# Performance work log

Hardware: AMD Instinct MI355X
Metric: run time of the kernel (lower is better)

The kernel has to match this reference:

```python
import jax, jax.numpy as jnp
import numpy as np

B, N, C = 16, 32768, 3
PRE, POST, IOU_THRESH = 4096, 512, 0.7


def setup_inputs() -> dict:
    key = jax.random.key(0)
    k1, k2, k3, k4 = jax.random.split(key, 4)
    centers = jax.random.uniform(k1, (B, N, 3), minval=0.0, maxval=70.0)
    sizes = jax.random.uniform(k2, (B, N, 3), minval=1.0, maxval=5.0)
    ry = jax.random.uniform(k3, (B, N, 1), minval=-np.pi, maxval=np.pi)
    batch_box_preds = jnp.concatenate([centers, sizes, ry], axis=-1)  # (B,N,7)
    batch_cls_preds = jax.random.uniform(k4, (B, N, C))  # normalized class scores
    return {"batch_box_preds": batch_box_preds, "batch_cls_preds": batch_cls_preds}


def _nms_single(boxes, scores):
    """Greedy class-agnostic NMS for one sample.
    boxes: (N,7) [x,y,z,dx,dy,dz,ry]; scores: (N,).
    Returns selected indices into the original N boxes and a validity mask,
    both of fixed length POST (padded).
    BEV IoU uses axis-aligned footprints (x,y,dx,dy)."""
    top_s, top_i = jax.lax.top_k(scores, PRE)  # pre-maxsize filtering by score
    tb = boxes[top_i]  # (PRE,7)
    x1 = tb[:, 0] - tb[:, 3] * 0.5
    x2 = tb[:, 0] + tb[:, 3] * 0.5
    y1 = tb[:, 1] - tb[:, 4] * 0.5
    y2 = tb[:, 1] + tb[:, 4] * 0.5
    area = (x2 - x1) * (y2 - y1)

    def step(active, _):
        ms = jnp.where(active, top_s, -jnp.inf)
        j = jnp.argmax(ms)
        valid = active[j]
        ix = jnp.clip(jnp.minimum(x2, x2[j]) - jnp.maximum(x1, x1[j]), 0.0)
        iy = jnp.clip(jnp.minimum(y2, y2[j]) - jnp.maximum(y1, y1[j]), 0.0)
        inter = ix * iy
        iou = inter / (area + area[j] - inter + 1e-8)
        # suppress overlapping boxes (j suppresses itself, iou==1)
        active = active & jnp.where(valid, iou < IOU_THRESH, True)
        return active, (jnp.where(valid, top_i[j], 0), valid)

    active0 = jnp.ones(PRE, dtype=bool)
    _, (sel_idx, sel_valid) = jax.lax.scan(step, active0, None, length=POST)
    return sel_idx, sel_valid


def reference(batch_box_preds, batch_cls_preds):
    # cur_roi_scores, cur_roi_labels = torch.max(cls_preds, dim=1)
    scores = jnp.max(batch_cls_preds, axis=-1)          # (B,N)
    labels = jnp.argmax(batch_cls_preds, axis=-1)       # (B,N)
    sel_idx, sel_valid = jax.vmap(_nms_single)(batch_box_preds, scores)  # (B,POST)
    gather = jax.vmap(lambda a, i: a[i])
    rois = jnp.where(sel_valid[..., None], gather(batch_box_preds, sel_idx), 0.0)  # (B,POST,7)
    roi_scores = jnp.where(sel_valid, gather(scores, sel_idx), 0.0)                # (B,POST)
    roi_labels = jnp.where(sel_valid, gather(labels, sel_idx), 0) + 1              # (B,POST), pad -> 1 as in torch code
    return rois, roi_scores, roi_labels
```

## Files before the change

### kernel.cpp

```cpp
#include <hip/hip_runtime.h>
#include <stdint.h>

#define BATCH 16
#define NBOX  32768
#define PRE   4096
#define POST  512

#define PADIDX(i) ((i) + ((i) >> 4))

typedef unsigned long long u64;
typedef unsigned int u32;
typedef unsigned short u16;

__device__ inline u64 shfl64(u64 v, int src) {
    int lo = __shfl((int)(v & 0xffffffffULL), src);
    int hi = __shfl((int)(v >> 32), src);
    return ((u64)(u32)hi << 32) | (u32)lo;
}

__global__ __launch_bounds__(1024) void k_sortkeys4096(const float* __restrict__ cls,
                                                       u64* __restrict__ out) {
    __shared__ u64 s[PRE + (PRE >> 4)];
    int g = blockIdx.x;
    u64* dst = out + (size_t)g * PRE;
    int tid = threadIdx.x;
    for (int i = tid; i < PRE; i += 1024) {
        int idx = g * PRE + i;
        const float* c = cls + (size_t)idx * 3;
        float sc = fmaxf(fmaxf(c[0], c[1]), c[2]);
        u32 sb = __float_as_uint(sc);
        s[PADIDX(i)] = ((u64)(~sb) << 32) | (u32)(idx & (NBOX - 1));
    }
    for (int k = 2; k <= PRE; k <<= 1) {
        for (int jj = k >> 1; jj > 0; jj >>= 1) {
            __syncthreads();
            for (int p = tid; p < PRE / 2; p += 1024) {
                int i = 2 * p - (p & (jj - 1));
                int l = i + jj;
                bool asc = ((i & k) == 0);
                u64 a = s[PADIDX(i)], b = s[PADIDX(l)];
                if ((a > b) == asc) { s[PADIDX(i)] = b; s[PADIDX(l)] = a; }
            }
        }
    }
    __syncthreads();
    for (int i = tid; i < PRE; i += 1024) dst[i] = s[PADIDX(i)];
}

__global__ __launch_bounds__(256) void k_mergepath(const u64* __restrict__ in,
                                                   u64* __restrict__ out, int npairs) {
    __shared__ u64 sA[PRE], sB[PRE];
    int b = blockIdx.x / npairs, p = blockIdx.x % npairs;
    const u64* A  = in + ((size_t)b * npairs * 2 + (size_t)p * 2) * PRE;
    const u64* Bp = A + PRE;
    u64* dst = out + ((size_t)b * npairs + p) * PRE;
    int tid = threadIdx.x;
    for (int i = tid; i < PRE; i += 256) { sA[i] = A[i]; sB[i] = Bp[i]; }
    __syncthreads();
    int d = tid * 16;
    int lo = d > PRE ? d - PRE : 0;
    int hi = d < PRE ? d : PRE;
    while (lo < hi) {
        int mid = (lo + hi) >> 1;
        if (sA[mid] < sB[d - 1 - mid]) lo = mid + 1; else hi = mid;
    }
    int a = lo, bi = d - lo;
    u64 av = a  < PRE ? sA[a]  : ~0ULL;
    u64 bv = bi < PRE ? sB[bi] : ~0ULL;
    u64 res[16];
    #pragma unroll
    for (int q = 0; q < 16; ++q) {
        bool ta = av < bv;
        res[q] = ta ? av : bv;
        if (ta) { ++a;  av = a  < PRE ? sA[a]  : ~0ULL; }
        else    { ++bi; bv = bi < PRE ? sB[bi] : ~0ULL; }
    }
    #pragma unroll
    for (int q = 0; q < 16; ++q) dst[d + q] = res[q];
}

__global__ __launch_bounds__(256) void k_coords(const u64* __restrict__ topkeys,
                                                const float* __restrict__ boxes,
                                                float* __restrict__ cx1,
                                                float* __restrict__ cy1,
                                                float* __restrict__ cx2,
                                                float* __restrict__ cy2,
                                                float* __restrict__ car) {
    int g = blockIdx.x * 256 + threadIdx.x;
    int b = g >> 12;
    u64 key = topkeys[g];
    int n = (int)(key & 0xffffffffULL);
    const float* bp = boxes + ((size_t)b * NBOX + n) * 7;
    float cx = bp[0], cy = bp[1], dx = bp[3], dy = bp[4];
    float hx = __fmul_rn(dx, 0.5f), hy = __fmul_rn(dy, 0.5f);
    float x1 = __fsub_rn(cx, hx), x2 = __fadd_rn(cx, hx);
    float y1 = __fsub_rn(cy, hy), y2 = __fadd_rn(cy, hy);
    cx1[g] = x1; cy1[g] = y1; cx2[g] = x2; cy2[g] = y2;
    car[g] = __fmul_rn(__fsub_rn(x2, x1), __fsub_rn(y2, y1));
}

__global__ __launch_bounds__(256) void k_iou(const float* __restrict__ cx1,
                                             const float* __restrict__ cy1,
                                             const float* __restrict__ cx2,
                                             const float* __restrict__ cy2,
                                             const float* __restrict__ car,
                                             u32* __restrict__ counts,
                                             u16* __restrict__ lists,
                                             u32* __restrict__ spcnt,
                                             u32* __restrict__ spill) {
    __shared__ float s1[64], s2[64], s3[64], s4[64], s5[64];
    int b = blockIdx.y;
    int t = blockIdx.x, blk = 0;
    while (t >= 64 - blk) { t -= 64 - blk; ++blk; }
    int wd = blk + t;
    size_t base = (size_t)b * PRE;
    int bb = b * PRE;
    int tid = threadIdx.x;
    if (tid < 64) {
        int i = blk * 64 + tid;
        s1[tid] = cx1[base + i]; s2[tid] = cy1[base + i];
        s3[tid] = cx2[base + i]; s4[tid] = cy2[base + i];
        s5[tid] = car[base + i];
    }
    __syncthreads();
    int w = tid >> 6, lane = tid & 63;
    int j = wd * 64 + lane;
    float jx1 = cx1[base + j], jy1 = cy1[base + j];
    float jx2 = cx2[base + j], jy2 = cy2[base + j];
    float ja  = car[base + j];
    const double M = (double)0.7f - 0x1p-25;
    int r0 = w * 16;
    #pragma unroll 4
    for (int r = 0; r < 16; ++r) {
        int i = blk * 64 + r0 + r;
        float rx1 = s1[r0 + r], ry1 = s2[r0 + r];
        float rx2 = s3[r0 + r], ry2 = s4[r0 + r], ra = s5[r0 + r];
        float ix = fmaxf(__fsub_rn(fminf(jx2, rx2), fmaxf(jx1, rx1)), 0.0f);
        float iy = fmaxf(__fsub_rn(fminf(jy2, ry2), fmaxf(jy1, ry1)), 0.0f);
        float inter = __fmul_rn(ix, iy);
        bool cand = (j > i) && (inter > 0.0f);
        u64 m = 0;
        if (__ballot(cand)) {
            float ssum = __fadd_rn(ja, ra);
            float d    = __fsub_rn(ssum, inter);
            float q    = __fadd_rn(d, 1e-8f);
            bool sup = cand && ((double)inter > M * (double)q);
            m = __ballot(sup);
        }
        if (lane == 0 && m) {
            u64 mm = m;
            while (mm) {
                int jj = __ffsll(mm) - 1; mm &= mm - 1;
                u32 slot = atomicAdd(&counts[bb + i], 1u);
                if (slot < 7)
                    lists[((size_t)(bb + i)) * 8 + 1 + slot] = (u16)(wd * 64 + jj);
                else {
                    u32 sp = atomicAdd(&spcnt[b], 1u);
                    if (sp < 4096) spill[(b << 12) + sp] = ((u32)i << 16) | (u32)(wd * 64 + jj);
                }
            }
        }
    }
}

__global__ __launch_bounds__(256) void k_walk(const u32* __restrict__ counts,
                                              const u16* __restrict__ lists,
                                              const u32* __restrict__ spcnt,
                                              const u32* __restrict__ spill,
                                              const u64* __restrict__ topkeys,
                                              const float* __restrict__ boxes,
                                              const float* __restrict__ cls,
                                              float* __restrict__ out) {
    __shared__ uint4 lrow[PRE];
    __shared__ u32   lbits[128];
    __shared__ u32   lspill[4096];
    __shared__ int   ssel[POST];
    __shared__ int   scnt, ssp;
    int b = blockIdx.x;
    int tid = threadIdx.x;
    const u64* keys = topkeys + (size_t)b * PRE;
    const uint4* listv = (const uint4*)(lists + ((size_t)b * PRE) * 8);

    if (tid < 128) lbits[tid] = 0;
    if (tid == 0) { u32 s = spcnt[b]; ssp = s > 4096u ? 4096 : (int)s; }
    __syncthreads();
    for (int i = tid; i < PRE; i += 256) {
        uint4 row = listv[i];
        u32 c = counts[b * PRE + i];
        row.x = (row.x & 0xFFFF0000u) | (c > 65535u ? 65535u : c);
        lrow[i] = row;
        if (c) atomicOr(&lbits[i >> 5], 1u << (i & 31));
    }
    __syncthreads();
    int spn = ssp;
    for (int q = tid; q < spn; q += 256) lspill[q] = spill[(b << 12) + q];
    __syncthreads();

    if (tid < 64) {
        int lane = tid;
        u64 act = ~0ULL;
        u64 hasl = ((u64)lbits[2 * lane + 1] << 32) | lbits[2 * lane];
        int cnt = 0;
        while (true) {
            u64 bal = __ballot(act != 0ULL);
            if (!bal) break;
            int fw = __ffsll(bal) - 1;
            u64 wsel = shfl64(act, fw);
            int i = (fw << 6) + __ffsll(wsel) - 1;
            if (lane == 0) ssel[cnt] = i;
            if (++cnt == POST) break;
            if (lane == fw) act &= ~(1ULL << (i & 63));
            u64 hb = shfl64(hasl, fw);
            if ((hb >> (i & 63)) & 1ULL) {
                uint4 row = lrow[i];
                int c = (int)(row.x & 0xFFFFu);
                u64 m = 0;
                int e;
                e = (int)(row.x >> 16);      if (c > 0 && (e >> 6) == lane) m |= 1ULL << (e & 63);
                e = (int)(row.y & 0xFFFFu);  if (c > 1 && (e >> 6) == lane) m |= 1ULL << (e & 63);
                e = (int)(row.y >> 16);      if (c > 2 && (e >> 6) == lane) m |= 1ULL << (e & 63);
                e = (int)(row.z & 0xFFFFu);  if (c > 3 && (e >> 6) == lane) m |= 1ULL << (e & 63);
                e = (int)(row.z >> 16);      if (c > 4 && (e >> 6) == lane) m |= 1ULL << (e & 63);
                e = (int)(row.w & 0xFFFFu);  if (c > 5 && (e >> 6) == lane) m |= 1ULL << (e & 63);
                e = (int)(row.w >> 16);      if (c > 6 && (e >> 6) == lane) m |= 1ULL << (e & 63);
                if (c > 7) {
                    for (int q = 0; q < spn; ++q) {
                        u32 en = lspill[q];
                        if ((int)(en >> 16) == i) {
                            int j2 = (int)(en & 0xFFFFu);
                            if ((j2 >> 6) == lane) m |= 1ULL << (j2 & 63);
                        }
                    }
                }
                act &= ~m;
            }
        }
        if (lane == 0) scnt = cnt;
    }
    __syncthreads();
    int cnt = scnt;
    for (int k = tid; k < POST; k += 256) if (k >= cnt) ssel[k] = -1;
    __syncthreads();

    const int R1 = BATCH * POST * 7;
    const int R2 = R1 + BATCH * POST;
    for (int k = tid; k < POST; k += 256) {
        int j = ssel[k];
        float* ro = out + ((size_t)b * POST + k) * 7;
        float score = 0.0f, labelf = 1.0f;
        if (j >= 0) {
            u64 key = keys[j];
            int n = (int)(key & 0xffffffffULL);
            const float* bp = boxes + ((size_t)b * NBOX + n) * 7;
            #pragma unroll
            for (int c = 0; c < 7; ++c) ro[c] = bp[c];
            score = __uint_as_float(~(u32)(key >> 32));
            const float* cp = cls + ((size_t)b * NBOX + n) * 3;
            float c0 = cp[0], c1 = cp[1], c2 = cp[2];
            int lab = 0; float best = c0;
            if (c1 > best) { best = c1; lab = 1; }
            if (c2 > best) { lab = 2; }
            labelf = (float)(lab + 1);
        } else {
            #pragma unroll
            for (int c = 0; c < 7; ++c) ro[c] = 0.0f;
        }
        out[R1 + b * POST + k] = score;
        out[R2 + b * POST + k] = labelf;
    }
}

__global__ __launch_bounds__(1024) void k_nms(const u64* __restrict__ topkeys,
                                              const float* __restrict__ boxes,
                                              const float* __restrict__ cls,
                                              float* __restrict__ out) {
    __shared__ float sx1[PRE], sy1[PRE], sx2[PRE], sy2[PRE], sarea[PRE];
    __shared__ int   sorig[PRE];
    __shared__ u64   smask[PRE / 64];
    __shared__ int   ssel[POST];
    __shared__ int   scur;
    int b = blockIdx.x;
    int tid = threadIdx.x;
    const u64* keys = topkeys + (size_t)b * PRE;

    for (int i = tid; i < PRE; i += 1024) {
        u64 key = keys[i];
        int n = (int)(key & 0xffffffffULL);
        sorig[i] = n;
        const float* bp = boxes + ((size_t)b * NBOX + n) * 7;
        float cx = bp[0], cy = bp[1], dx = bp[3], dy = bp[4];
        float hx = __fmul_rn(dx, 0.5f), hy = __fmul_rn(dy, 0.5f);
        float x1 = __fsub_rn(cx, hx), x2 = __fadd_rn(cx, hx);
        float y1 = __fsub_rn(cy, hy), y2 = __fadd_rn(cy, hy);
        sx1[i] = x1; sx2[i] = x2; sy1[i] = y1; sy2[i] = y2;
        sarea[i] = __fmul_rn(__fsub_rn(x2, x1), __fsub_rn(y2, y1));
    }
    if (tid < PRE / 64) smask[tid] = ~0ULL;
    __syncthreads();

    int lane = tid & 63;
    int wv   = tid >> 6;
    for (int r = 0; r < POST; ++r) {
        if (tid < 64) {
            u64 w = smask[lane];
            u64 nz = __ballot(w != 0ULL);
            int j = -1;
            if (nz) {
                int fw = __ffsll(nz) - 1;
                u64 wf = shfl64(w, fw);
                j = (fw << 6) + __ffsll(wf) - 1;
            }
            if (lane == 0) { scur = j; ssel[r] = j; }
        }
        __syncthreads();
        int j = scur;
        if (j < 0) {
            for (int k = r + tid; k < POST; k += 1024) ssel[k] = -1;
            __syncthreads();
            break;
        }
        float x1j = sx1[j], x2j = sx2[j], y1j = sy1[j], y2j = sy2[j], aj = sarea[j];
        for (int wd = wv * 4; wd < wv * 4 + 4; ++wd) {
            u64 m = smask[wd];
            if (m == 0ULL) continue;
            int i = (wd << 6) + lane;
            float ix = fmaxf(__fsub_rn(fminf(sx2[i], x2j), fmaxf(sx1[i], x1j)), 0.0f);
            float iy = fmaxf(__fsub_rn(fminf(sy2[i], y2j), fmaxf(sy1[i], y1j)), 0.0f);
            float inter = __fmul_rn(ix, iy);
            float denom = __fadd_rn(__fsub_rn(__fadd_rn(sarea[i], aj), inter), 1e-8f);
            float iou = __fdiv_rn(inter, denom);
            u64 clr = __ballot(!(iou < 0.7f));
            if (lane == 0) smask[wd] = m & ~clr;
        }
        __syncthreads();
    }

    const int R1 = BATCH * POST * 7;
    const int R2 = R1 + BATCH * POST;
    for (int k = tid; k < POST; k += 1024) {
        int j = ssel[k];
        float* ro = out + ((size_t)b * POST + k) * 7;
        float score = 0.0f, labelf = 1.0f;
        if (j >= 0) {
            int n = sorig[j];
            const float* bp = boxes + ((size_t)b * NBOX + n) * 7;
            #pragma unroll
            for (int c = 0; c < 7; ++c) ro[c] = bp[c];
            u64 key = keys[j];
            score = __uint_as_float(~(u32)(key >> 32));
            const float* cp = cls + ((size_t)b * NBOX + n) * 3;
            float c0 = cp[0], c1 = cp[1], c2 = cp[2];
            int lab = 0; float best = c0;
            if (c1 > best) { best = c1; lab = 1; }
            if (c2 > best) { lab = 2; }
            labelf = (float)(lab + 1);
        } else {
            #pragma unroll
            for (int c = 0; c < 7; ++c) ro[c] = 0.0f;
        }
        out[R1 + b * POST + k] = score;
        out[R2 + b * POST + k] = labelf;
    }
}

extern "C" void kernel_launch(void* const* d_in, const int* in_sizes, int n_in,
                              void* d_out, int out_size, void* d_ws, size_t ws_size,
                              hipStream_t stream) {
    const float* boxes = (const float*)d_in[0];
    const float* cls   = (const float*)d_in[1];
    float* out = (float*)d_out;

    char* ws = (char*)d_ws;
    u64*   keysA  = (u64*)(ws + 0);
    u64*   keysB  = (u64*)(ws + 4194304);
    float* cx1    = (float*)(ws + 8388608);
    float* cy1    = (float*)(ws + 8650752);
    float* cx2    = (float*)(ws + 8912896);
    float* cy2    = (float*)(ws + 9175040);
    float* car    = (float*)(ws + 9437184);
    u32*   counts = (u32*)(ws + 9699328);
    u32*   spcnt  = (u32*)(ws + 9961472);
    u32*   spill  = (u32*)(ws + 9961536);
    u16*   lists  = (u16*)(ws + 10223680);
    const size_t NEED = 10223680 + (size_t)BATCH * PRE * 8 * sizeof(u16);

    k_sortkeys4096<<<BATCH * 8, 1024, 0, stream>>>(cls, keysB);
    k_mergepath<<<BATCH * 4, 256, 0, stream>>>(keysB, keysA, 4);
    k_mergepath<<<BATCH * 2, 256, 0, stream>>>(keysA, keysB, 2);
    k_mergepath<<<BATCH, 256, 0, stream>>>(keysB, keysA, 1);

    if (ws_size >= NEED) {
        hipMemsetAsync(ws + 9699328, 0, 262208, stream);
        k_coords<<<(BATCH * PRE) / 256, 256, 0, stream>>>(keysA, boxes,
                                                          cx1, cy1, cx2, cy2, car);
        k_iou<<<dim3(2080, BATCH), 256, 0, stream>>>(cx1, cy1, cx2, cy2, car,
                                                     counts, lists, spcnt, spill);
        k_walk<<<BATCH, 256, 0, stream>>>(counts, lists, spcnt, spill,
                                          keysA, boxes, cls, out);
    } else {
        k_nms<<<BATCH, 1024, 0, stream>>>(keysA, boxes, cls, out);
    }
}
```

Before: 310.6 us.

## Run greedy NMS walk on a single thread with shared-memory suppression masks

The greedy selection walk moves from a 64-lane wavefront that used ballot and shuffle for every pick to one thread scanning 64-bit words of an active mask kept in LDS. Suppression inside the current word clears bits in a register, and suppression in later words uses atomicAnd on shared memory. The aim is to remove the per-iteration cross-lane ballot and shuffle latency in this serial loop. The cost is that one thread now does every step, and it takes a shared-memory round trip whenever a suppressed box lies in another word.

```diff
diff --git a/kernel.cpp b/kernel.cpp
--- a/kernel.cpp
+++ b/kernel.cpp
@@ -172,7 +172,8 @@
                                               const float* __restrict__ cls,
                                               float* __restrict__ out) {
     __shared__ uint4 lrow[PRE];
-    __shared__ u32   lbits[128];
+    __shared__ u64   smask[64];
+    __shared__ u64   haslw[64];
     __shared__ u32   lspill[4096];
     __shared__ int   ssel[POST];
     __shared__ int   scnt, ssp;
@@ -181,7 +182,7 @@
     const u64* keys = topkeys + (size_t)b * PRE;
     const uint4* listv = (const uint4*)(lists + ((size_t)b * PRE) * 8);
 
-    if (tid < 128) lbits[tid] = 0;
+    if (tid < 64) { smask[tid] = ~0ULL; haslw[tid] = 0ULL; }
     if (tid == 0) { u32 s = spcnt[b]; ssp = s > 4096u ? 4096 : (int)s; }
     __syncthreads();
     for (int i = tid; i < PRE; i += 256) {
@@ -189,53 +190,54 @@
         u32 c = counts[b * PRE + i];
         row.x = (row.x & 0xFFFF0000u) | (c > 65535u ? 65535u : c);
         lrow[i] = row;
-        if (c) atomicOr(&lbits[i >> 5], 1u << (i & 31));
+        if (c) atomicOr(&haslw[i >> 6], 1ULL << (i & 63));
     }
     __syncthreads();
     int spn = ssp;
     for (int q = tid; q < spn; q += 256) lspill[q] = spill[(b << 12) + q];
     __syncthreads();
 
-    if (tid < 64) {
-        int lane = tid;
-        u64 act = ~0ULL;
-        u64 hasl = ((u64)lbits[2 * lane + 1] << 32) | lbits[2 * lane];
+    if (tid == 0) {
         int cnt = 0;
-        while (true) {
-            u64 bal = __ballot(act != 0ULL);
-            if (!bal) break;
-            int fw = __ffsll(bal) - 1;
-            u64 wsel = shfl64(act, fw);
-            int i = (fw << 6) + __ffsll(wsel) - 1;
-            if (lane == 0) ssel[cnt] = i;
-            if (++cnt == POST) break;
-            if (lane == fw) act &= ~(1ULL << (i & 63));
-            u64 hb = shfl64(hasl, fw);
-            if ((hb >> (i & 63)) & 1ULL) {
-                uint4 row = lrow[i];
-                int c = (int)(row.x & 0xFFFFu);
-                u64 m = 0;
-                int e;
-                e = (int)(row.x >> 16);      if (c > 0 && (e >> 6) == lane) m |= 1ULL << (e & 63);
-                e = (int)(row.y & 0xFFFFu);  if (c > 1 && (e >> 6) == lane) m |= 1ULL << (e & 63);
-                e = (int)(row.y >> 16);      if (c > 2 && (e >> 6) == lane) m |= 1ULL << (e & 63);
-                e = (int)(row.z & 0xFFFFu);  if (c > 3 && (e >> 6) == lane) m |= 1ULL << (e & 63);
-                e = (int)(row.z >> 16);      if (c > 4 && (e >> 6) == lane) m |= 1ULL << (e & 63);
-                e = (int)(row.w & 0xFFFFu);  if (c > 5 && (e >> 6) == lane) m |= 1ULL << (e & 63);
-                e = (int)(row.w >> 16);      if (c > 6 && (e >> 6) == lane) m |= 1ULL << (e & 63);
-                if (c > 7) {
-                    for (int q = 0; q < spn; ++q) {
-                        u32 en = lspill[q];
-                        if ((int)(en >> 16) == i) {
-                            int j2 = (int)(en & 0xFFFFu);
-                            if ((j2 >> 6) == lane) m |= 1ULL << (j2 & 63);
+        for (int wd = 0; wd < 64 && cnt < POST; ++wd) {
+            asm volatile("s_waitcnt lgkmcnt(0)" ::: "memory");
+            u64 w  = smask[wd];
+            u64 hl = haslw[wd];
+            while (w) {
+                int t = __ffsll(w) - 1;
+                w &= w - 1;
+                int i = (wd << 6) + t;
+                ssel[cnt++] = i;
+                if (cnt == POST) break;
+                if ((hl >> t) & 1ULL) {
+                    uint4 row = lrow[i];
+                    int c = (int)(row.x & 0xFFFFu);
+                    int e;
+                    #define APPLY(e) do { \
+                        if ((e >> 6) == wd) w &= ~(1ULL << (e & 63)); \
+                        else atomicAnd(&smask[e >> 6], ~(1ULL << (e & 63))); \
+                    } while (0)
+                    e = (int)(row.x >> 16);     if (c > 0) APPLY(e);
+                    e = (int)(row.y & 0xFFFFu); if (c > 1) APPLY(e);
+                    e = (int)(row.y >> 16);     if (c > 2) APPLY(e);
+                    e = (int)(row.z & 0xFFFFu); if (c > 3) APPLY(e);
+                    e = (int)(row.z >> 16);     if (c > 4) APPLY(e);
+                    e = (int)(row.w & 0xFFFFu); if (c > 5) APPLY(e);
+                    e = (int)(row.w >> 16);     if (c > 6) APPLY(e);
+                    if (c > 7) {
+                        for (int q = 0; q < spn; ++q) {
+                            u32 en = lspill[q];
+                            if ((int)(en >> 16) == i) {
+                                int e2 = (int)(en & 0xFFFFu);
+                                APPLY(e2);
+                            }
                         }
                     }
+                    #undef APPLY
                 }
-                act &= ~m;
             }
         }
-        if (lane == 0) scnt = cnt;
+        scnt = cnt;
     }
     __syncthreads();
     int cnt = scnt;
```

After: 266.4 us. -14.2%, faster.
